# Kernel optimization log

Measured on AMD Instinct MI355X. Metric: run time of the kernel, lower is better.

## Reference

```python
import jax, jax.numpy as jnp
import numpy as np

EPS = 1e-5

def layer_norm(x, g, b):
    mu = jnp.mean(x, axis=-1, keepdims=True)
    var = jnp.mean(jnp.square(x - mu), axis=-1, keepdims=True)
    return (x - mu) * jax.lax.rsqrt(var + EPS) * g + b

def gather_recent(seq_tokens, seq_mask, count):
    # vectorized right-aligned gather of last `count` valid tokens per row
    B, S, D = seq_tokens.shape
    csum = jnp.cumsum(seq_mask.astype(jnp.int32), axis=1)          # [B,S]
    total = csum[:, -1:]                                           # [B,1]
    rank = total - csum                                            # 0 = last valid (at valid positions)
    sel = seq_mask & (rank < count)
    dest = jnp.where(sel, count - 1 - rank, count)                 # dump invalid into slot `count`
    b_idx = jnp.arange(B)[:, None]
    buf = jnp.zeros((B, count + 1, D), seq_tokens.dtype)
    recent = buf.at[b_idx, dest].set(seq_tokens * sel[..., None].astype(seq_tokens.dtype))[:, :count]
    recent_mask = jnp.arange(count)[None, :] >= (count - total)    # [B,count]
    return recent, recent_mask

def setup_inputs() -> dict:
    key = jax.random.key(0)
    B, S, D, H, P = 16, 2048, 1024, 16, 8
    ks = jax.random.split(key, 8)
    hidden_states = jax.random.normal(ks[0], (B, S, D), jnp.float32)
    lengths = jax.random.randint(ks[1], (B,), 1, S + 1)
    valid_mask = jnp.arange(S)[None, :] < lengths[:, None]
    s = 0.02
    return {
        "hidden_states": hidden_states,
        "valid_mask": valid_mask,
        "queries": jax.random.normal(ks[2], (P, D), jnp.float32) * s,
        "in_proj_w": jax.random.normal(ks[3], (3 * D, D), jnp.float32) * s,
        "in_proj_b": jnp.zeros((3 * D,), jnp.float32),
        "out_w": jax.random.normal(ks[4], (D, D), jnp.float32) * s,
        "out_b": jnp.zeros((D,), jnp.float32),
        "ln_pma_g": jnp.ones((D,), jnp.float32),
        "ln_pma_b": jnp.zeros((D,), jnp.float32),
        "ln_v_g": jnp.ones((D,), jnp.float32),
        "ln_v_b": jnp.zeros((D,), jnp.float32),
        "W_v": jax.random.normal(ks[5], (D, D), jnp.float32) * s,
        "b_v": jnp.zeros((D,), jnp.float32),
        "ln_g_g": jnp.ones((D,), jnp.float32),
        "ln_g_b": jnp.zeros((D,), jnp.float32),
        "W_g": jax.random.normal(ks[6], (D, D), jnp.float32) * s,
        "b_g": jnp.zeros((D,), jnp.float32),
        "cls_count": 1, "pma_count": 8, "recent_count": 64, "num_heads": 16,
    }

def reference(hidden_states, valid_mask, queries, in_proj_w, in_proj_b, out_w, out_b,
              ln_pma_g, ln_pma_b, ln_v_g, ln_v_b, W_v, b_v, ln_g_g, ln_g_b, W_g, b_g,
              cls_count, pma_count, recent_count, num_heads):
    B, S, D = hidden_states.shape
    H = num_heads
    hd = D // H
    # ---- PMA (torch nn.MultiheadAttention, batch_first, eval/no-dropout) ----
    Wq, Wk, Wv_ = in_proj_w[:D], in_proj_w[D:2 * D], in_proj_w[2 * D:]
    bq, bk, bv_ = in_proj_b[:D], in_proj_b[D:2 * D], in_proj_b[2 * D:]
    q = (queries @ Wq.T + bq)                       # [P, D]
    k = hidden_states @ Wk.T + bk                   # [B, S, D]
    v = hidden_states @ Wv_.T + bv_                 # [B, S, D]
    qh = q.reshape(pma_count, H, hd)                # [P, H, hd]
    kh = k.reshape(B, S, H, hd)
    vh = v.reshape(B, S, H, hd)
    scores = jnp.einsum('phd,bshd->bhps', qh, kh) / jnp.sqrt(jnp.asarray(hd, hidden_states.dtype))
    scores = jnp.where(valid_mask[:, None, None, :], scores, jnp.asarray(-1e9, scores.dtype))
    attn = jax.nn.softmax(scores, axis=-1)          # [B, H, P, S]
    ctx = jnp.einsum('bhps,bshd->bphd', attn, vh).reshape(B, pma_count, D)
    pooled = ctx @ out_w.T + out_b
    pma_tokens = layer_norm(queries[None, :, :] + pooled, ln_pma_g, ln_pma_b)  # [B, P, D]
    pma_mask = jnp.ones((B, pma_count), bool)
    # ---- split cls / sequence, gather recent ----
    cls_tokens = hidden_states[:, :cls_count]
    cls_mask = valid_mask[:, :cls_count]
    recent_tokens, recent_mask = gather_recent(hidden_states[:, cls_count:],
                                               valid_mask[:, cls_count:], recent_count)
    summary = jnp.concatenate([cls_tokens, pma_tokens, recent_tokens], axis=1)
    summary_mask = jnp.concatenate([cls_mask, pma_mask, recent_mask], axis=1)
    # ---- SiLU self-gating ----
    val = jax.nn.silu(layer_norm(summary, ln_v_g, ln_v_b) @ W_v.T + b_v)
    gate = jax.nn.sigmoid(layer_norm(summary, ln_g_g, ln_g_b) @ W_g.T + b_g)
    gated = gate * val * summary_mask[..., None].astype(summary.dtype)
    return gated, summary_mask
```

## Files before the change

### kernel.cpp

```cpp
#include <hip/hip_runtime.h>
#include <hip/hip_bf16.h>
#include <math.h>


#define Bn 16
#define Sn 2048
#define Dn 1024
#define Hn 16
#define Pn 8
#define Tn 73
#define RECn 64

typedef __attribute__((ext_vector_type(8))) short short8;
typedef __attribute__((ext_vector_type(4))) float f32x4;

__device__ __forceinline__ short f2bf(float x) {
    union { __hip_bfloat16 h; short s; } u;
    u.h = __float2bfloat16(x);
    return u.s;
}

__device__ __forceinline__ int swzP(int row, int ks, int pitch) {
    return row * pitch + (ks ^ ((row & 7) << 3));
}

__global__ void detect_mask_kernel(const unsigned char* __restrict__ raw,
                                   int* __restrict__ flag) {
    __shared__ int any;
    if (threadIdx.x == 0) any = 0;
    __syncthreads();
    const uint4* r4 = (const uint4*)raw;
    int local = 0;
    for (int i = threadIdx.x; i < (Bn * Sn) / 16; i += blockDim.x) {
        uint4 w = r4[i];
        if ((w.x & 0xFFFFFF00u) | (w.y & 0xFFFFFF00u) |
            (w.z & 0xFFFFFF00u) | (w.w & 0xFFFFFF00u)) local = 1;
    }
    if (local) any = 1;
    __syncthreads();
    if (threadIdx.x == 0) *flag = any;
}

__global__ void canon_mask_kernel(const void* __restrict__ raw,
                                  const int* __restrict__ flag,
                                  unsigned char* __restrict__ canon) {
    int i = blockIdx.x * blockDim.x + threadIdx.x;
    if (i >= Bn * Sn) return;
    unsigned char v;
    if (*flag)
        v = ((const unsigned char*)raw)[i] ? 1 : 0;
    else
        v = ((const int*)raw)[i] ? 1 : 0;
    canon[i] = v;
}

__global__ void prep_kernel(const unsigned char* __restrict__ valid,
                            int* __restrict__ totals, int* __restrict__ rsrc,
                            float* __restrict__ maskf) {
    int b = blockIdx.x, t = threadIdx.x;
    const int SP = Sn - 1;
    __shared__ int lc[256];
    if (t < RECn) rsrc[b * RECn + t] = -1;

    int base = t * 8;
    unsigned char m[8];
    int cnt = 0;
#pragma unroll
    for (int i = 0; i < 8; i++) {
        int idx = base + i;
        m[i] = (idx < SP) ? valid[(size_t)b * Sn + 1 + idx] : (unsigned char)0;
        cnt += m[i] ? 1 : 0;
    }
    lc[t] = cnt;
    __syncthreads();
    for (int off = 1; off < 256; off <<= 1) {
        int add = (t >= off) ? lc[t - off] : 0;
        __syncthreads();
        lc[t] += add;
        __syncthreads();
    }
    int total = lc[255];
    int run = lc[t] - cnt;
#pragma unroll
    for (int i = 0; i < 8; i++) {
        if (m[i]) {
            run++;
            int rank = total - run;
            if (rank < RECn) rsrc[b * RECn + (RECn - 1 - rank)] = base + i + 1;
        }
    }
    if (t == 0) totals[b] = total;
    if (t < Tn) {
        float mv;
        if (t == 0) mv = valid[(size_t)b * Sn] ? 1.0f : 0.0f;
        else if (t < 1 + Pn) mv = 1.0f;
        else mv = ((t - 9) >= RECn - total) ? 1.0f : 0.0f;
        maskf[b * Tn + t] = mv;
    }
}

__global__ void q_kernel(const float* __restrict__ queries,
                         const float* __restrict__ in_w,
                         const float* __restrict__ in_b,
                         float* __restrict__ q) {
    int wid = (blockIdx.x * blockDim.x + threadIdx.x) >> 6;
    int lane = threadIdx.x & 63;
    if (wid >= Pn * Dn) return;
    int p = wid >> 10, j = wid & 1023;
    float acc = 0.0f;
    for (int c = lane; c < Dn; c += 64)
        acc += queries[p * Dn + c] * in_w[(size_t)j * Dn + c];
#pragma unroll
    for (int off = 32; off > 0; off >>= 1) acc += __shfl_down(acc, off);
    if (lane == 0) q[wid] = acc + in_b[j];
}

__global__ void A_kernel(const float* __restrict__ q,
                         const float* __restrict__ in_w,
                         const float* __restrict__ in_b,
                         short* __restrict__ Amat_bf, float* __restrict__ c0) {
    int h = blockIdx.x, cblk = blockIdx.y;
    int c = cblk * 256 + threadIdx.x;
    __shared__ float qs[8][64];
    for (int i = threadIdx.x; i < 512; i += 256) {
        int p = i >> 6, d = i & 63;
        qs[p][d] = q[p * Dn + h * 64 + d];
    }
    __syncthreads();
    float acc[8] = {};
#pragma unroll 8
    for (int d = 0; d < 64; d++) {
        float w = in_w[(size_t)(Dn + h * 64 + d) * Dn + c];
#pragma unroll
        for (int p = 0; p < 8; p++) acc[p] = fmaf(qs[p][d], w, acc[p]);
    }
#pragma unroll
    for (int p = 0; p < 8; p++)
        Amat_bf[(size_t)(h * 8 + p) * Dn + c] = f2bf(acc[p] * 0.125f);
    if (cblk == 0 && threadIdx.x < 8) {
        int p = threadIdx.x;
        float a = 0.0f;
        for (int d = 0; d < 64; d++) a += qs[p][d] * in_b[Dn + h * 64 + d];
        c0[h * 8 + p] = a * 0.125f;
    }
}

__global__ void wcvt_kernel(const float* __restrict__ w, short* __restrict__ wbf, int n) {
    int i = (blockIdx.x * blockDim.x + threadIdx.x) * 8;
    if (i >= n) return;
    f32x4 x0 = *(const f32x4*)(w + i);
    f32x4 x1 = *(const f32x4*)(w + i + 4);
    short8 o;
#pragma unroll
    for (int j = 0; j < 4; j++) { o[j] = f2bf(x0[j]); o[j + 4] = f2bf(x1[j]); }
    *(short8*)(wbf + i) = o;
}

__global__ __launch_bounds__(512) void scores_mfma(const float* __restrict__ hidden,
                                                   const short* __restrict__ Amat_bf,
                                                   const float* __restrict__ c0,
                                                   const unsigned char* __restrict__ valid,
                                                   float* __restrict__ scores) {
    __shared__ short Bsh[2][64 * 512];
    int tid = threadIdx.x, wave = tid >> 6, lane = tid & 63;
    int l15 = lane & 15, q = lane >> 4;
    int m0 = blockIdx.x * 128 + wave * 16;
    int b = m0 >> 11, s_base = m0 & 2047;

    int sr = tid >> 2, skc = (tid & 3) * 64;
    const short* aglob = Amat_bf + (size_t)sr * Dn + skc;

    {
#pragma unroll
        for (int j = 0; j < 8; j++) {
            short8 v = *(const short8*)(aglob + j * 8);
            *(short8*)(&Bsh[0][swzP(sr, skc + j * 8, 256)]) = v;
        }
    }
    __syncthreads();

    const float* aptr = hidden + (size_t)(m0 + l15) * Dn + q * 8;
    f32x4 acc[8] = {};
    f32x4 pa[4][2];
#pragma unroll
    for (int d = 0; d < 4; d++) {
        pa[d][0] = *(const f32x4*)(aptr + d * 32);
        pa[d][1] = *(const f32x4*)(aptr + d * 32 + 4);
    }

    for (int kq = 0; kq < 4; kq++) {
        int cur = kq & 1;
        short8 sreg[8];
        if (kq < 3) {
            const short* src = aglob + (kq + 1) * 256;
#pragma unroll
            for (int j = 0; j < 8; j++) sreg[j] = *(const short8*)(src + j * 8);
        }
#pragma unroll
        for (int icq = 0; icq < 8; icq++) {
            int ic = kq * 8 + icq;
            f32x4 h0 = pa[icq & 3][0], h1 = pa[icq & 3][1];
            if (ic + 4 < 32) {
                pa[icq & 3][0] = *(const f32x4*)(aptr + (ic + 4) * 32);
                pa[icq & 3][1] = *(const f32x4*)(aptr + (ic + 4) * 32 + 4);
            }
            short8 av;
#pragma unroll
            for (int i = 0; i < 4; i++) { av[i] = f2bf(h0[i]); av[i + 4] = f2bf(h1[i]); }
#pragma unroll
            for (int nt = 0; nt < 8; nt++) {
                short8 bv = *(const short8*)(&Bsh[cur][swzP(nt * 16 + l15, icq * 32 + q * 8, 256)]);
                acc[nt] = __builtin_amdgcn_mfma_f32_16x16x32_bf16(av, bv, acc[nt], 0, 0, 0);
            }
        }
        if (kq < 3) {
            __syncthreads();
#pragma unroll
            for (int j = 0; j < 8; j++)
                *(short8*)(&Bsh[cur ^ 1][swzP(sr, skc + j * 8, 256)]) = sreg[j];
            __syncthreads();
        }
    }

    int srow = s_base + q * 4;
    const unsigned char* vptr = valid + (size_t)b * Sn + srow;
    bool ok0 = vptr[0] != 0, ok1 = vptr[1] != 0, ok2 = vptr[2] != 0, ok3 = vptr[3] != 0;
#pragma unroll
    for (int nt = 0; nt < 8; nt++) {
        int hp = nt * 16 + l15;
        float cc = c0[hp];
        f32x4 st;
        st[0] = ok0 ? acc[nt][0] + cc : -1.0e9f;
        st[1] = ok1 ? acc[nt][1] + cc : -1.0e9f;
        st[2] = ok2 ? acc[nt][2] + cc : -1.0e9f;
        st[3] = ok3 ? acc[nt][3] + cc : -1.0e9f;
        *(f32x4*)(scores + (size_t)(b * 128 + hp) * Sn + srow) = st;
    }
}

__global__ __launch_bounds__(256) void softmax_kernel(const float* __restrict__ scores,
                                                      short* __restrict__ attn_bf) {
    const float* row = scores + (size_t)blockIdx.x * Sn;
    short* orow = attn_bf + (size_t)blockIdx.x * Sn;
    int t = threadIdx.x;
    __shared__ float red[256];
    f32x4 v0 = *(const f32x4*)(row + t * 8);
    f32x4 v1 = *(const f32x4*)(row + t * 8 + 4);
    float mx = -1.0e30f;
#pragma unroll
    for (int i = 0; i < 4; i++) { mx = fmaxf(mx, v0[i]); mx = fmaxf(mx, v1[i]); }
    red[t] = mx;
    __syncthreads();
    for (int off = 128; off > 0; off >>= 1) {
        if (t < off) red[t] = fmaxf(red[t], red[t + off]);
        __syncthreads();
    }
    mx = red[0];
    __syncthreads();
    float e[8];
    float sum = 0.0f;
#pragma unroll
    for (int i = 0; i < 4; i++) {
        e[i] = expf(v0[i] - mx); sum += e[i];
        e[i + 4] = expf(v1[i] - mx); sum += e[i + 4];
    }
    red[t] = sum;
    __syncthreads();
    for (int off = 128; off > 0; off >>= 1) {
        if (t < off) red[t] += red[t + off];
        __syncthreads();
    }
    float inv = 1.0f / red[0];
    short8 o;
#pragma unroll
    for (int i = 0; i < 8; i++) o[i] = f2bf(e[i] * inv);
    *(short8*)(orow + t * 8) = o;
}

__global__ __launch_bounds__(512) void U_mfma(const short* __restrict__ attn_bf,
                                              const float* __restrict__ hidden,
                                              float* __restrict__ Up0,
                                              float* __restrict__ Up1,
                                              float* __restrict__ Up2,
                                              float* __restrict__ Up3) {
    __shared__ short Hs[64 * 512];
    int n0 = blockIdx.x * 64, b = blockIdx.y, z = blockIdx.z;
    int zbase = z * 512;
    float* Up = (z == 0) ? Up0 : (z == 1) ? Up1 : (z == 2) ? Up2 : Up3;
    int tid = threadIdx.x, wave = tid >> 6, lane = tid & 63;
    int l15 = lane & 15, q = lane >> 4;

    {
        const float* src = hidden + ((size_t)b * Sn + zbase + tid) * Dn + n0;
#pragma unroll
        for (int c8 = 0; c8 < 64; c8 += 8) {
            f32x4 x = *(const f32x4*)(src + c8);
            f32x4 y = *(const f32x4*)(src + c8 + 4);
#pragma unroll
            for (int i = 0; i < 4; i++) {
                int c = c8 + i;
                Hs[c * 512 + (tid ^ ((c & 7) << 3))] = f2bf(x[i]);
            }
#pragma unroll
            for (int i = 0; i < 4; i++) {
                int c = c8 + 4 + i;
                Hs[c * 512 + (tid ^ ((c & 7) << 3))] = f2bf(y[i]);
            }
        }
    }
    __syncthreads();

    const short* ap = attn_bf + ((size_t)b * 128 + wave * 16 + l15) * Sn + zbase + q * 8;
    f32x4 acc[4] = {};
    short8 pa4[4];
#pragma unroll
    for (int d = 0; d < 4; d++) pa4[d] = *(const short8*)(ap + d * 32);
#pragma unroll
    for (int ic = 0; ic < 16; ic++) {
        short8 av = pa4[ic & 3];
        if (ic + 4 < 16) pa4[ic & 3] = *(const short8*)(ap + (ic + 4) * 32);
#pragma unroll
        for (int nf = 0; nf < 4; nf++) {
            short8 bv = *(const short8*)(&Hs[swzP(nf * 16 + l15, ic * 32 + q * 8, 512)]);
            acc[nf] = __builtin_amdgcn_mfma_f32_16x16x32_bf16(av, bv, acc[nf], 0, 0, 0);
        }
    }
    int hp = wave * 16 + q * 4;
#pragma unroll
    for (int nf = 0; nf < 4; nf++) {
        int c = n0 + nf * 16 + l15;
        float* up = Up + (size_t)(b * 128 + hp) * Dn + c;
#pragma unroll
        for (int r = 0; r < 4; r++) up[(size_t)r * Dn] = acc[nf][r];
    }
}

__global__ __launch_bounds__(64) void ctx_mfma(const float* __restrict__ Up0,
                                               const float* __restrict__ Up1,
                                               const float* __restrict__ Up2,
                                               const float* __restrict__ Up3,
                                               const float* __restrict__ in_w,
                                               const float* __restrict__ in_b,
                                               float* __restrict__ ctx) {
    int bh = blockIdx.x, b = bh >> 4, h = bh & 15;
    int lane = threadIdx.x & 63, l15 = lane & 15, koff = (lane >> 4) * 8;
    int p = l15 & 7;
    size_t uoff = ((size_t)b * 128 + h * 8 + p) * Dn + koff;
    const float* wv = in_w + (size_t)(2 * Dn + h * 64 + l15) * Dn + koff;
    f32x4 acc[4] = {};
    for (int k0 = 0; k0 < Dn; k0 += 32) {
        f32x4 a0 = *(const f32x4*)(Up0 + uoff + k0);
        f32x4 a1 = *(const f32x4*)(Up0 + uoff + k0 + 4);
        f32x4 b0 = *(const f32x4*)(Up1 + uoff + k0);
        f32x4 b1 = *(const f32x4*)(Up1 + uoff + k0 + 4);
        f32x4 d0 = *(const f32x4*)(Up2 + uoff + k0);
        f32x4 d1 = *(const f32x4*)(Up2 + uoff + k0 + 4);
        f32x4 e0 = *(const f32x4*)(Up3 + uoff + k0);
        f32x4 e1 = *(const f32x4*)(Up3 + uoff + k0 + 4);
        short8 av;
#pragma unroll
        for (int i = 0; i < 4; i++) {
            av[i] = f2bf((a0[i] + b0[i]) + (d0[i] + e0[i]));
            av[i + 4] = f2bf((a1[i] + b1[i]) + (d1[i] + e1[i]));
        }
#pragma unroll
        for (int nt = 0; nt < 4; nt++) {
            f32x4 w0 = *(const f32x4*)(wv + (size_t)nt * 16 * Dn + k0);
            f32x4 w1 = *(const f32x4*)(wv + (size_t)nt * 16 * Dn + k0 + 4);
            short8 bv;
#pragma unroll
            for (int i = 0; i < 4; i++) { bv[i] = f2bf(w0[i]); bv[i + 4] = f2bf(w1[i]); }
            acc[nt] = __builtin_amdgcn_mfma_f32_16x16x32_bf16(av, bv, acc[nt], 0, 0, 0);
        }
    }
    if (lane < 32) {
        int prow = (lane >> 4) * 4;
#pragma unroll
        for (int nt = 0; nt < 4; nt++) {
            int d = h * 64 + nt * 16 + l15;
            float bias = in_b[2 * Dn + d];
#pragma unroll
            for (int r = 0; r < 4; r++)
                ctx[(size_t)(b * 8 + prow + r) * Dn + d] = acc[nt][r] + bias;
        }
    }
}

__global__ __launch_bounds__(256) void pooled_mfma(const float* __restrict__ A,
                                                   const float* __restrict__ B,
                                                   const float* __restrict__ bias,
                                                   float* __restrict__ C, int M) {
    int wave = threadIdx.x >> 6, lane = threadIdx.x & 63;
    int l15 = lane & 15, koff = (lane >> 4) * 8;
    int m0 = blockIdx.x * 64 + (wave >> 1) * 32;
    int n0 = blockIdx.y * 64 + (wave & 1) * 32;
    f32x4 acc[2][2] = {};
    int ra0 = min(m0 + l15, M - 1);
    int ra1 = min(m0 + 16 + l15, M - 1);
    const float* a0p = A + (size_t)ra0 * Dn + koff;
    const float* a1p = A + (size_t)ra1 * Dn + koff;
    const float* b0p = B + (size_t)(n0 + l15) * Dn + koff;
    const float* b1p = B + (size_t)(n0 + 16 + l15) * Dn + koff;
    for (int k0 = 0; k0 < Dn; k0 += 32) {
        short8 av0, av1, bv0, bv1;
        f32x4 x, y;
        x = *(const f32x4*)(a0p + k0); y = *(const f32x4*)(a0p + k0 + 4);
#pragma unroll
        for (int i = 0; i < 4; i++) { av0[i] = f2bf(x[i]); av0[i + 4] = f2bf(y[i]); }
        x = *(const f32x4*)(a1p + k0); y = *(const f32x4*)(a1p + k0 + 4);
#pragma unroll
        for (int i = 0; i < 4; i++) { av1[i] = f2bf(x[i]); av1[i + 4] = f2bf(y[i]); }
        x = *(const f32x4*)(b0p + k0); y = *(const f32x4*)(b0p + k0 + 4);
#pragma unroll
        for (int i = 0; i < 4; i++) { bv0[i] = f2bf(x[i]); bv0[i + 4] = f2bf(y[i]); }
        x = *(const f32x4*)(b1p + k0); y = *(const f32x4*)(b1p + k0 + 4);
#pragma unroll
        for (int i = 0; i < 4; i++) { bv1[i] = f2bf(x[i]); bv1[i + 4] = f2bf(y[i]); }
        acc[0][0] = __builtin_amdgcn_mfma_f32_16x16x32_bf16(av0, bv0, acc[0][0], 0, 0, 0);
        acc[0][1] = __builtin_amdgcn_mfma_f32_16x16x32_bf16(av0, bv1, acc[0][1], 0, 0, 0);
        acc[1][0] = __builtin_amdgcn_mfma_f32_16x16x32_bf16(av1, bv0, acc[1][0], 0, 0, 0);
        acc[1][1] = __builtin_amdgcn_mfma_f32_16x16x32_bf16(av1, bv1, acc[1][1], 0, 0, 0);
    }
#pragma unroll
    for (int mf = 0; mf < 2; mf++) {
        int row0 = m0 + mf * 16 + (lane >> 4) * 4;
#pragma unroll
        for (int nf = 0; nf < 2; nf++) {
            int col = n0 + nf * 16 + l15;
            float bval = bias[col];
#pragma unroll
            for (int r = 0; r < 4; r++) {
                int row = row0 + r;
                if (row < M) C[(size_t)row * Dn + col] = acc[mf][nf][r] + bval;
            }
        }
    }
}

__global__ __launch_bounds__(256) void wgemm_mfma(const short* __restrict__ Abf,
                                                  const short* __restrict__ Bbf,
                                                  const float* __restrict__ bias,
                                                  float* __restrict__ C, int M) {
    int wave = threadIdx.x >> 6, lane = threadIdx.x & 63;
    int m0 = blockIdx.x * 64 + (wave >> 1) * 32;
    int n0 = blockIdx.y * 64 + (wave & 1) * 32;
    int koff = (lane >> 4) * 8;
    f32x4 acc[2][2] = {};
    int ra0 = min(m0 + (lane & 15), M - 1);
    int ra1 = min(m0 + 16 + (lane & 15), M - 1);
    const short* a0p = Abf + (size_t)ra0 * Dn + koff;
    const short* a1p = Abf + (size_t)ra1 * Dn + koff;
    const short* b0p = Bbf + (size_t)(n0 + (lane & 15)) * Dn + koff;
    const short* b1p = Bbf + (size_t)(n0 + 16 + (lane & 15)) * Dn + koff;
    for (int k0 = 0; k0 < Dn; k0 += 32) {
        short8 av0 = *(const short8*)(a0p + k0);
        short8 av1 = *(const short8*)(a1p + k0);
        short8 bv0 = *(const short8*)(b0p + k0);
        short8 bv1 = *(const short8*)(b1p + k0);
        acc[0][0] = __builtin_amdgcn_mfma_f32_16x16x32_bf16(av0, bv0, acc[0][0], 0, 0, 0);
        acc[0][1] = __builtin_amdgcn_mfma_f32_16x16x32_bf16(av0, bv1, acc[0][1], 0, 0, 0);
        acc[1][0] = __builtin_amdgcn_mfma_f32_16x16x32_bf16(av1, bv0, acc[1][0], 0, 0, 0);
        acc[1][1] = __builtin_amdgcn_mfma_f32_16x16x32_bf16(av1, bv1, acc[1][1], 0, 0, 0);
    }
#pragma unroll
    for (int mf = 0; mf < 2; mf++) {
        int row0 = m0 + mf * 16 + (lane >> 4) * 4;
#pragma unroll
        for (int nf = 0; nf < 2; nf++) {
            int col = n0 + nf * 16 + (lane & 15);
            float bval = bias[col];
#pragma unroll
            for (int r = 0; r < 4; r++) {
                int row = row0 + r;
                if (row < M) C[(size_t)row * Dn + col] = acc[mf][nf][r] + bval;
            }
        }
    }
}

__device__ __forceinline__ float block_sum(float v, float* red) {
    int tid = threadIdx.x;
    red[tid] = v;
    __syncthreads();
    for (int off = 128; off > 0; off >>= 1) {
        if (tid < off) red[tid] += red[tid + off];
        __syncthreads();
    }
    float r = red[0];
    __syncthreads();
    return r;
}

__global__ void summary_ln_kernel(const float* __restrict__ hidden,
                                  const float* __restrict__ queries,
                                  const float* __restrict__ pooled,
                                  const int* __restrict__ rsrc,
                                  const float* __restrict__ gpma, const float* __restrict__ bpma,
                                  const float* __restrict__ gv, const float* __restrict__ bv,
                                  const float* __restrict__ gg, const float* __restrict__ bg,
                                  short* __restrict__ lnv, short* __restrict__ lng) {
    __shared__ float red[256];
    int b = blockIdx.x, t = blockIdx.y, tid = threadIdx.x;
    float x[4];
    if (t == 0) {
#pragma unroll
        for (int i = 0; i < 4; i++)
            x[i] = hidden[(size_t)b * Sn * Dn + tid + i * 256];
    } else if (t < 1 + Pn) {
        int p = t - 1;
#pragma unroll
        for (int i = 0; i < 4; i++) {
            int c = tid + i * 256;
            x[i] = queries[p * Dn + c] + pooled[((size_t)b * Pn + p) * Dn + c];
        }
    } else {
        int src = rsrc[b * RECn + (t - 9)];
        if (src >= 0) {
#pragma unroll
            for (int i = 0; i < 4; i++)
                x[i] = hidden[((size_t)b * Sn + src) * Dn + tid + i * 256];
        } else {
#pragma unroll
            for (int i = 0; i < 4; i++) x[i] = 0.0f;
        }
    }
    if (t >= 1 && t < 1 + Pn) {
        float mu = block_sum(x[0] + x[1] + x[2] + x[3], red) * (1.0f / Dn);
        float d2 = 0.0f;
#pragma unroll
        for (int i = 0; i < 4; i++) { float d = x[i] - mu; d2 += d * d; }
        float inv = rsqrtf(block_sum(d2, red) * (1.0f / Dn) + 1e-5f);
#pragma unroll
        for (int i = 0; i < 4; i++) {
            int c = tid + i * 256;
            x[i] = (x[i] - mu) * inv * gpma[c] + bpma[c];
        }
    }
    float mu = block_sum(x[0] + x[1] + x[2] + x[3], red) * (1.0f / Dn);
    float d2 = 0.0f;
#pragma unroll
    for (int i = 0; i < 4; i++) { float d = x[i] - mu; d2 += d * d; }
    float inv = rsqrtf(block_sum(d2, red) * (1.0f / Dn) + 1e-5f);
    size_t row = (size_t)(b * Tn + t) * Dn;
#pragma unroll
    for (int i = 0; i < 4; i++) {
        int c = tid + i * 256;
        float xh = (x[i] - mu) * inv;
        lnv[row + c] = f2bf(xh * gv[c] + bv[c]);
        lng[row + c] = f2bf(xh * gg[c] + bg[c]);
    }
}

__global__ void gated_kernel(const float* __restrict__ c1, const float* __restrict__ c2,
                             const float* __restrict__ maskf, float* __restrict__ out) {
    int gi = blockIdx.x * blockDim.x + threadIdx.x;
    int row = gi >> 10;
    float m = maskf[row];
    float a = c1[gi], g = c2[gi];
    float sv = a / (1.0f + expf(-a));
    float sg = 1.0f / (1.0f + expf(-g));
    out[gi] = sg * sv * m;
}

extern "C" void kernel_launch(void* const* d_in, const int* in_sizes, int n_in,
                              void* d_out, int out_size, void* d_ws, size_t ws_size,
                              hipStream_t stream) {
    const float* hidden = (const float*)d_in[0];
    const void* valid_raw = d_in[1];
    const float* queries = (const float*)d_in[2];
    const float* in_w = (const float*)d_in[3];
    const float* in_b = (const float*)d_in[4];
    const float* out_w = (const float*)d_in[5];
    const float* out_b = (const float*)d_in[6];
    const float* ln_pma_g = (const float*)d_in[7];
    const float* ln_pma_b = (const float*)d_in[8];
    const float* ln_v_g = (const float*)d_in[9];
    const float* ln_v_b = (const float*)d_in[10];
    const float* W_v = (const float*)d_in[11];
    const float* b_v = (const float*)d_in[12];
    const float* ln_g_g = (const float*)d_in[13];
    const float* ln_g_b = (const float*)d_in[14];
    const float* W_g = (const float*)d_in[15];
    const float* b_g = (const float*)d_in[16];

    float* ws = (float*)d_ws;
    float* out = (float*)d_out;

    float* SC      = ws;
    short* attn_bf = (short*)(ws + 4194304);
    float* Up0     = ws;
    float* Up1     = ws + 2097152;
    float* Up2     = ws + 6291456;
    float* Up3     = ws + 8388608;
    float* qbuf    = ws + 10485760;
    short* Amat_bf = (short*)(ws + 10493952);
    float* c0      = ws + 10559488;
    float* ctx     = ws + 10559744;
    float* pooled  = ws + 10690816;
    short* Wv_bf   = (short*)(ws + 10821888);
    short* Wg_bf   = (short*)(ws + 11346176);
    int*   ivals   = (int*)(ws + 11870464);
    int* totals = ivals;
    int* rsrc = ivals + 16;
    int* flag = ivals + 16 + 1024;
    unsigned char* canon = (unsigned char*)(ivals + 16 + 1024 + 16);
    short* lnv_bf = (short*)ws;
    short* lng_bf = (short*)(ws + 622592);
    float* c1 = ws + 1245184;
    float* c2 = ws + 2441216;
    float* maskf = out + (size_t)Bn * Tn * Dn;

    const int M2 = Bn * Tn;

    detect_mask_kernel<<<1, 256, 0, stream>>>((const unsigned char*)valid_raw, flag);
    canon_mask_kernel<<<(Bn * Sn) / 256, 256, 0, stream>>>(valid_raw, flag, canon);
    prep_kernel<<<Bn, 256, 0, stream>>>(canon, totals, rsrc, maskf);
    q_kernel<<<(Pn * Dn) / 4, 256, 0, stream>>>(queries, in_w, in_b, qbuf);
    A_kernel<<<dim3(Hn, 4), 256, 0, stream>>>(qbuf, in_w, in_b, Amat_bf, c0);
    wcvt_kernel<<<512, 256, 0, stream>>>(W_v, Wv_bf, Dn * Dn);
    wcvt_kernel<<<512, 256, 0, stream>>>(W_g, Wg_bf, Dn * Dn);
    scores_mfma<<<(Bn * Sn) / 128, 512, 0, stream>>>(hidden, Amat_bf, c0, canon, SC);
    softmax_kernel<<<Bn * 128, 256, 0, stream>>>(SC, attn_bf);
    U_mfma<<<dim3(16, Bn, 4), 512, 0, stream>>>(attn_bf, hidden, Up0, Up1, Up2, Up3);
    ctx_mfma<<<Bn * Hn, 64, 0, stream>>>(Up0, Up1, Up2, Up3, in_w, in_b, ctx);
    pooled_mfma<<<dim3(2, 16), 256, 0, stream>>>(ctx, out_w, out_b, pooled, Bn * Pn);
    summary_ln_kernel<<<dim3(Bn, Tn), 256, 0, stream>>>(hidden, queries, pooled, rsrc,
                                                        ln_pma_g, ln_pma_b, ln_v_g, ln_v_b,
                                                        ln_g_g, ln_g_b, lnv_bf, lng_bf);
    wgemm_mfma<<<dim3((M2 + 63) / 64, 16), 256, 0, stream>>>(lnv_bf, Wv_bf, b_v, c1, M2);
    wgemm_mfma<<<dim3((M2 + 63) / 64, 16), 256, 0, stream>>>(lng_bf, Wg_bf, b_g, c2, M2);
    gated_kernel<<<(Bn * Tn * Dn) / 256, 256, 0, stream>>>(c1, c2, maskf, out);
}
```

Measured before the change: 254.1 us.

## Restructure scores GEMM with direct global-to-LDS loads and 2x2 wave tiling

Rewrites the scores kernel so that both the fp32 hidden tile and the bf16 A-matrix slices are streamed into swizzled, double-buffered LDS through global_load_lds. Blocks now hold 64 rows with 4 waves tiled 2x2 over rows and heads, and step K in chunks of 32. Previously each wave pulled hidden rows into registers and every block loaded a large slab of the A matrix. The aim is to cut register pressure and LDS footprint and to let loads overlap compute. The cost is a barrier on every K step and 32 small iterations, each with little compute.

New measurement: 249.3 us. No clear change (-1.9%).

```diff
diff --git a/kernel.cpp b/kernel.cpp
--- a/kernel.cpp
+++ b/kernel.cpp
@@ -18,6 +18,11 @@
     union { __hip_bfloat16 h; short s; } u;
     u.h = __float2bfloat16(x);
     return u.s;
+}
+
+__device__ __forceinline__ void gload_lds16(const void* g, void* l) {
+    __builtin_amdgcn_global_load_lds((const __attribute__((address_space(1))) void*)g,
+                                     (__attribute__((address_space(3))) void*)l, 16, 0, 0);
 }
 
 __device__ __forceinline__ int swzP(int row, int ks, int pitch) {
@@ -156,85 +161,81 @@
     *(short8*)(wbf + i) = o;
 }
 
-__global__ __launch_bounds__(512) void scores_mfma(const float* __restrict__ hidden,
+__global__ __launch_bounds__(256) void scores_mfma(const float* __restrict__ hidden,
                                                    const short* __restrict__ Amat_bf,
                                                    const float* __restrict__ c0,
                                                    const unsigned char* __restrict__ valid,
                                                    float* __restrict__ scores) {
-    __shared__ short Bsh[2][64 * 512];
+    __shared__ float Af[2][64 * 32];
+    __shared__ short Bs[2][128 * 32];
     int tid = threadIdx.x, wave = tid >> 6, lane = tid & 63;
     int l15 = lane & 15, q = lane >> 4;
-    int m0 = blockIdx.x * 128 + wave * 16;
+    int m0 = blockIdx.x * 64;
     int b = m0 >> 11, s_base = m0 & 2047;
-
-    int sr = tid >> 2, skc = (tid & 3) * 64;
-    const short* aglob = Amat_bf + (size_t)sr * Dn + skc;
-
-    {
-#pragma unroll
-        for (int j = 0; j < 8; j++) {
-            short8 v = *(const short8*)(aglob + j * 8);
-            *(short8*)(&Bsh[0][swzP(sr, skc + j * 8, 256)]) = v;
-        }
-    }
-    __syncthreads();
-
-    const float* aptr = hidden + (size_t)(m0 + l15) * Dn + q * 8;
-    f32x4 acc[8] = {};
-    f32x4 pa[4][2];
-#pragma unroll
-    for (int d = 0; d < 4; d++) {
-        pa[d][0] = *(const f32x4*)(aptr + d * 32);
-        pa[d][1] = *(const f32x4*)(aptr + d * 32 + 4);
-    }
-
-    for (int kq = 0; kq < 4; kq++) {
-        int cur = kq & 1;
-        short8 sreg[8];
-        if (kq < 3) {
-            const short* src = aglob + (kq + 1) * 256;
-#pragma unroll
-            for (int j = 0; j < 8; j++) sreg[j] = *(const short8*)(src + j * 8);
-        }
-#pragma unroll
-        for (int icq = 0; icq < 8; icq++) {
-            int ic = kq * 8 + icq;
-            f32x4 h0 = pa[icq & 3][0], h1 = pa[icq & 3][1];
-            if (ic + 4 < 32) {
-                pa[icq & 3][0] = *(const f32x4*)(aptr + (ic + 4) * 32);
-                pa[icq & 3][1] = *(const f32x4*)(aptr + (ic + 4) * 32 + 4);
-            }
-            short8 av;
-#pragma unroll
-            for (int i = 0; i < 4; i++) { av[i] = f2bf(h0[i]); av[i + 4] = f2bf(h1[i]); }
-#pragma unroll
-            for (int nt = 0; nt < 8; nt++) {
-                short8 bv = *(const short8*)(&Bsh[cur][swzP(nt * 16 + l15, icq * 32 + q * 8, 256)]);
-                acc[nt] = __builtin_amdgcn_mfma_f32_16x16x32_bf16(av, bv, acc[nt], 0, 0, 0);
-            }
-        }
-        if (kq < 3) {
-            __syncthreads();
-#pragma unroll
-            for (int j = 0; j < 8; j++)
-                *(short8*)(&Bsh[cur ^ 1][swzP(sr, skc + j * 8, 256)]) = sreg[j];
-            __syncthreads();
-        }
-    }
-
-    int srow = s_base + q * 4;
-    const unsigned char* vptr = valid + (size_t)b * Sn + srow;
-    bool ok0 = vptr[0] != 0, ok1 = vptr[1] != 0, ok2 = vptr[2] != 0, ok3 = vptr[3] != 0;
-#pragma unroll
-    for (int nt = 0; nt < 8; nt++) {
-        int hp = nt * 16 + l15;
-        float cc = c0[hp];
-        f32x4 st;
-        st[0] = ok0 ? acc[nt][0] + cc : -1.0e9f;
-        st[1] = ok1 ? acc[nt][1] + cc : -1.0e9f;
-        st[2] = ok2 ? acc[nt][2] + cc : -1.0e9f;
-        st[3] = ok3 ? acc[nt][3] + cc : -1.0e9f;
-        *(f32x4*)(scores + (size_t)(b * 128 + hp) * Sn + srow) = st;
+    int ws = wave >> 1, wh = wave & 1;
+    int s0 = ws * 32, hp0 = wh * 64;
+
+    auto stage = [&](int bb, int k0) {
+#pragma unroll
+        for (int u = 0; u < 2; u++) {
+            int i = tid + u * 256;
+            int s = i >> 3, j = (i & 7) ^ (s & 7);
+            gload_lds16(hidden + (size_t)(m0 + s) * Dn + k0 + j * 4, &Af[bb][i * 4]);
+        }
+#pragma unroll
+        for (int u = 0; u < 2; u++) {
+            int i = tid + u * 256;
+            int hp = i >> 2, qq = (i & 3) ^ ((hp >> 1) & 3);
+            gload_lds16(Amat_bf + (size_t)hp * Dn + k0 + qq * 8, &Bs[bb][i * 8]);
+        }
+    };
+
+    f32x4 acc[2][4] = {};
+    stage(0, 0);
+    __syncthreads();
+
+    for (int t = 0; t < 32; t++) {
+        int bb = t & 1;
+        if (t + 1 < 32) stage(bb ^ 1, (t + 1) * 32);
+        short8 av[2], bv[4];
+#pragma unroll
+        for (int f = 0; f < 2; f++) {
+            int s = s0 + f * 16 + l15;
+            int base = s * 8;
+            f32x4 lo = *(const f32x4*)&Af[bb][(base + ((2 * q) ^ (s & 7))) * 4];
+            f32x4 hi = *(const f32x4*)&Af[bb][(base + ((2 * q + 1) ^ (s & 7))) * 4];
+#pragma unroll
+            for (int i = 0; i < 4; i++) { av[f][i] = f2bf(lo[i]); av[f][i + 4] = f2bf(hi[i]); }
+        }
+#pragma unroll
+        for (int f = 0; f < 4; f++) {
+            int hp = hp0 + f * 16 + l15;
+            bv[f] = *(const short8*)&Bs[bb][(hp * 4 + (q ^ ((hp >> 1) & 3))) * 8];
+        }
+#pragma unroll
+        for (int fa = 0; fa < 2; fa++)
+#pragma unroll
+            for (int fb = 0; fb < 4; fb++)
+                acc[fa][fb] = __builtin_amdgcn_mfma_f32_16x16x32_bf16(av[fa], bv[fb], acc[fa][fb], 0, 0, 0);
+        __syncthreads();
+    }
+
+#pragma unroll
+    for (int fa = 0; fa < 2; fa++) {
+        int srow = s_base + s0 + fa * 16 + q * 4;
+        const unsigned char* vptr = valid + (size_t)b * Sn + srow;
+        bool ok0 = vptr[0] != 0, ok1 = vptr[1] != 0, ok2 = vptr[2] != 0, ok3 = vptr[3] != 0;
+#pragma unroll
+        for (int fb = 0; fb < 4; fb++) {
+            int hp = hp0 + fb * 16 + l15;
+            float cc = c0[hp];
+            f32x4 st;
+            st[0] = ok0 ? acc[fa][fb][0] + cc : -1.0e9f;
+            st[1] = ok1 ? acc[fa][fb][1] + cc : -1.0e9f;
+            st[2] = ok2 ? acc[fa][fb][2] + cc : -1.0e9f;
+            st[3] = ok3 ? acc[fa][fb][3] + cc : -1.0e9f;
+            *(f32x4*)(scores + (size_t)(b * 128 + hp) * Sn + srow) = st;
+        }
     }
 }
 
@@ -619,7 +620,7 @@
     A_kernel<<<dim3(Hn, 4), 256, 0, stream>>>(qbuf, in_w, in_b, Amat_bf, c0);
     wcvt_kernel<<<512, 256, 0, stream>>>(W_v, Wv_bf, Dn * Dn);
     wcvt_kernel<<<512, 256, 0, stream>>>(W_g, Wg_bf, Dn * Dn);
-    scores_mfma<<<(Bn * Sn) / 128, 512, 0, stream>>>(hidden, Amat_bf, c0, canon, SC);
+    scores_mfma<<<(Bn * Sn) / 64, 256, 0, stream>>>(hidden, Amat_bf, c0, canon, SC);
     softmax_kernel<<<Bn * 128, 256, 0, stream>>>(SC, attn_bf);
     U_mfma<<<dim3(16, Bn, 4), 512, 0, stream>>>(attn_bf, hidden, Up0, Up1, Up2, Up3);
     ctx_mfma<<<Bn * Hn, 64, 0, stream>>>(Up0, Up1, Up2, Up3, in_w, in_b, ctx);
```
